# Performance work log

Measured on AMD Instinct MI355X. Metric: run time of the kernel, lower is better.

The kernel has to match this reference:

```python
import jax, jax.numpy as jnp
import numpy as np

GMIN, GMAX = 0.1, 1.0
DIMS = [3, 256, 256, 256, 1]

def setup_inputs() -> dict:
    key = jax.random.key(0)
    ks = jax.random.split(key, 12)
    inp = {"pos": jax.random.normal(ks[0], (1048576, 3), dtype=jnp.float32)}
    for i in range(4):
        fan_in = DIMS[i]
        bound = 1.0 / np.sqrt(fan_in)
        inp[f"W{i}"] = jax.random.uniform(ks[1 + 2 * i], (fan_in, DIMS[i + 1]), jnp.float32, -bound, bound)
        inp[f"b{i}"] = jax.random.uniform(ks[2 + 2 * i], (DIMS[i + 1],), jnp.float32, -bound, bound)
    for i in range(3):
        inp[f"sigma{i}"] = jax.random.uniform(ks[9 + i], (256,), jnp.float32, GMIN, GMAX)
    return inp

def _gauss(x, sigma):
    # Gaussian activation: exp(-x^2 / (2*sigma^2)), sigma learnable per-feature
    return jnp.exp(-jnp.square(x) / (2.0 * jnp.square(sigma)))

def _softplus8(x):
    # torch Softplus(beta=1, threshold=8): linear beyond threshold
    return jnp.where(x > 8.0, x, jnp.log1p(jnp.exp(jnp.minimum(x, 8.0))))

def reference(pos, W0, b0, W1, b1, W2, b2, W3, b3, sigma0, sigma1, sigma2):
    h = _gauss(pos @ W0 + b0, sigma0)      # [N,256]
    h = _gauss(h @ W1 + b1, sigma1)        # [N,256]
    h = _gauss(h @ W2 + b2, sigma2)        # [N,256]
    return _softplus8(h @ W3 + b3)         # [N,1]
```

## Files before the change

### kernel.cpp

```cpp
#include <hip/hip_runtime.h>
#include <hip/hip_bf16.h>

typedef __attribute__((ext_vector_type(8))) short short8;
typedef __attribute__((ext_vector_type(4))) float f32x4;
typedef __attribute__((ext_vector_type(2))) float f32x2;
typedef __attribute__((ext_vector_type(2))) unsigned int uint2v;

#define LOG2E 1.4426950408889634f
#define LN2   0.6931471805599453f

__device__ __forceinline__ unsigned short f2bf(float f) {
    union { float f; unsigned u; } v; v.f = f;
    unsigned u = v.u;
    u += 0x7fffu + ((u >> 16) & 1u);
    return (unsigned short)(u >> 16);
}
__device__ __forceinline__ float bf2f(unsigned short h) {
    union { unsigned u; float f; } v; v.u = ((unsigned)h) << 16;
    return v.f;
}
__device__ __forceinline__ unsigned pk_bf16(float a, float b) {
    __hip_bfloat162 t = __float22bfloat162_rn(float2{a, b});
    union { __hip_bfloat162 b; unsigned u; } v; v.b = t;
    return v.u;
}
__device__ __forceinline__ f32x2 pk_fma2(f32x2 a, f32x2 b, f32x2 c) {
    f32x2 d;
    asm("v_pk_fma_f32 %0, %1, %2, %3" : "=v"(d) : "v"(a), "v"(b), "v"(c));
    return d;
}

__global__ void pack_kernel(const float* __restrict__ W0, const float* __restrict__ W1,
                            const float* __restrict__ W2, const float* __restrict__ W3,
                            const float* __restrict__ s0, const float* __restrict__ s1,
                            const float* __restrict__ s2,
                            const float* __restrict__ b0, const float* __restrict__ b1,
                            const float* __restrict__ b2,
                            unsigned short* __restrict__ wp, float* __restrict__ negc) {
    int tid = blockIdx.x * 256 + threadIdx.x;
    if (tid < 8192) {
        int j = tid & 7, lane = (tid >> 3) & 63, ct = (tid >> 9) & 3, w = tid >> 11;
        int k = ((lane >> 4) * 8) + j;
        int n = w * 64 + 4 * (lane & 15) + ct;
        unsigned short v = 0;
        if (k < 9) {
            int d = k / 3, m = k - d * 3;
            float wv = W0[d * 256 + n];
            unsigned short wh = f2bf(wv);
            v = (m == 1) ? f2bf(wv - bf2f(wh)) : wh;
        }
        wp[tid] = v;
    } else if (tid < 139264) {
        int e = tid - 8192;
        const float* W = W1;
        if (e >= 65536) { W = W2; e -= 65536; }
        int j = e & 7, lane = (e >> 3) & 63, ct = (e >> 9) & 3, ks = (e >> 11) & 7, w = e >> 14;
        int k = ks * 32 + ((lane >> 4) * 8) + j;
        int n = w * 64 + 4 * (lane & 15) + ct;
        wp[tid] = f2bf(W[k * 256 + n]);
    } else if (tid < 143360) {
        int e = tid - 139264;
        int j = e & 7, lane = (e >> 3) & 63, ks = (e >> 9) & 1, w = e >> 10;
        int i16p = lane & 15, qp = lane >> 4;
        int k = w * 64 + ks * 32 + qp * 8 + j;
        float wv = W3[k];
        unsigned short wh = f2bf(wv);
        unsigned short v = 0;
        if (i16p == 0) v = wh;
        else if (i16p == 1) v = f2bf(wv - bf2f(wh));
        wp[139264 + e] = v;
    }
    if (tid < 768) {
        int l = tid >> 8, n = tid & 255;
        const float* s = (l == 0) ? s0 : (l == 1 ? s1 : s2);
        const float* b = (l == 0) ? b0 : (l == 1 ? b1 : b2);
        float sv = s[n], bv = b[n];
        float np = -LOG2E / (2.0f * sv * sv);
        negc[l * 768 + n]       = np;
        negc[l * 768 + 256 + n] = 2.0f * np * bv;
        negc[l * 768 + 512 + n] = np * bv * bv;
    }
}

constexpr int ROWS = 64;
constexpr int HSTR = 264;
constexpr int ASTR = 40;

template <int NKS, int SSTR>
__device__ __forceinline__ void layer(const unsigned short* __restrict__ src,
                                      const unsigned short* __restrict__ wpk,
                                      const float* __restrict__ ncp,
                                      unsigned short* __restrict__ hdst,
                                      int w, int i16, int q, bool presync) {
    f32x4 acc[4][4];
#pragma unroll
    for (int rg = 0; rg < 4; ++rg)
#pragma unroll
        for (int ct = 0; ct < 4; ++ct)
            acc[rg][ct] = f32x4{0.f, 0.f, 0.f, 0.f};

    const int lane = q * 16 + i16;
    const short8* wp8 = (const short8*)wpk + (w * NKS * 4) * 64 + lane;
    const unsigned short* abase = src + i16 * SSTR + q * 8;

    short8 wbufA[4], wbufB[4];
#pragma unroll
    for (int ct = 0; ct < 4; ++ct) wbufA[ct] = wp8[ct * 64];

#pragma unroll
    for (int ks = 0; ks < NKS; ++ks) {
        if (ks + 1 < NKS) {
#pragma unroll
            for (int ct = 0; ct < 4; ++ct) {
                short8 t = wp8[((ks + 1) * 4 + ct) * 64];
                if (ks & 1) wbufA[ct] = t; else wbufB[ct] = t;
            }
        }
        short8 a[4];
#pragma unroll
        for (int rg = 0; rg < 4; ++rg)
            a[rg] = *(const short8*)(abase + rg * 16 * SSTR + ks * 32);
#pragma unroll
        for (int ct = 0; ct < 4; ++ct) {
            short8 wf = (ks & 1) ? wbufB[ct] : wbufA[ct];
#pragma unroll
            for (int rg = 0; rg < 4; ++rg)
                acc[rg][ct] = __builtin_amdgcn_mfma_f32_16x16x32_bf16(a[rg], wf, acc[rg][ct], 0, 0, 0);
        }
    }

    const int ce = w * 64 + 4 * i16;
    const f32x4 np = *(const f32x4*)(ncp + ce);
    const f32x4 C1 = *(const f32x4*)(ncp + 256 + ce);
    const f32x4 C2 = *(const f32x4*)(ncp + 512 + ce);
    f32x2 npb[4], c1b[4], c2b[4];
#pragma unroll
    for (int ct = 0; ct < 4; ++ct) {
        npb[ct] = f32x2{np[ct], np[ct]};
        c1b[ct] = f32x2{C1[ct], C1[ct]};
        c2b[ct] = f32x2{C2[ct], C2[ct]};
    }
    uint2v av[4][4];
#pragma unroll
    for (int rg = 0; rg < 4; ++rg) {
        float gg[4][4];
#pragma unroll
        for (int ct = 0; ct < 4; ++ct) {
            f32x2 xlo = f32x2{acc[rg][ct][0], acc[rg][ct][1]};
            f32x2 xhi = f32x2{acc[rg][ct][2], acc[rg][ct][3]};
            f32x2 ulo = pk_fma2(npb[ct], xlo, c1b[ct]);
            f32x2 uhi = pk_fma2(npb[ct], xhi, c1b[ct]);
            f32x2 ylo = pk_fma2(ulo, xlo, c2b[ct]);
            f32x2 yhi = pk_fma2(uhi, xhi, c2b[ct]);
            gg[0][ct] = __builtin_amdgcn_exp2f(ylo[0]);
            gg[1][ct] = __builtin_amdgcn_exp2f(ylo[1]);
            gg[2][ct] = __builtin_amdgcn_exp2f(yhi[0]);
            gg[3][ct] = __builtin_amdgcn_exp2f(yhi[1]);
        }
#pragma unroll
        for (int rr = 0; rr < 4; ++rr) {
            uint2v v;
            v[0] = pk_bf16(gg[rr][0], gg[rr][1]);
            v[1] = pk_bf16(gg[rr][2], gg[rr][3]);
            av[rg][rr] = v;
        }
    }
    if (presync) __syncthreads();
#pragma unroll
    for (int rg = 0; rg < 4; ++rg) {
        int rbase = rg * 16 + q * 4;
#pragma unroll
        for (int rr = 0; rr < 4; ++rr)
            *(uint2v*)&hdst[(rbase + rr) * HSTR + ce] = av[rg][rr];
    }
    __syncthreads();
}

__global__ __launch_bounds__(256, 3) void mlp_kernel(
    const float* __restrict__ pos,
    const float* __restrict__ b3,
    const unsigned short* __restrict__ Wp,
    const float* __restrict__ negc,
    float* __restrict__ out)
{
    __shared__ unsigned short h[ROWS * HSTR];
    __shared__ unsigned short A0[ROWS * ASTR];

    const int tid  = threadIdx.x;
    const int lane = tid & 63;
    const int wave = tid >> 6;
    const int i16  = lane & 15, q = lane >> 4;
    const long row0 = (long)blockIdx.x * ROWS;

    if (tid < ROWS) {
        const float* pp = pos + (row0 + tid) * 3;
        float p0 = pp[0], p1 = pp[1], p2 = pp[2];
        short h0 = (short)f2bf(p0); short l0 = (short)f2bf(p0 - bf2f((unsigned short)h0));
        short h1 = (short)f2bf(p1); short l1 = (short)f2bf(p1 - bf2f((unsigned short)h1));
        short h2 = (short)f2bf(p2); short l2 = (short)f2bf(p2 - bf2f((unsigned short)h2));
        unsigned short* arow = A0 + tid * ASTR;
        *(short8*)(arow + 0)  = short8{h0, h0, l0, h1, h1, l1, h2, h2};
        *(short8*)(arow + 8)  = short8{l2, 0, 0, 0, 0, 0, 0, 0};
        *(short8*)(arow + 16) = short8{0, 0, 0, 0, 0, 0, 0, 0};
        *(short8*)(arow + 24) = short8{0, 0, 0, 0, 0, 0, 0, 0};
    }
    __syncthreads();

    layer<1, ASTR>(A0, Wp,         negc,        h, wave, i16, q, false);
    layer<8, HSTR>(h,  Wp + 8192,  negc + 768,  h, wave, i16, q, true);
    layer<8, HSTR>(h,  Wp + 73728, negc + 1536, h, wave, i16, q, true);

    {
        const short8* w3p = (const short8*)(Wp + 139264) + (wave * 2) * 64 + lane;
        const unsigned short* ab3 = h + i16 * HSTR + wave * 64 + q * 8;
        f32x4 acc3[4];
#pragma unroll
        for (int rg = 0; rg < 4; ++rg) acc3[rg] = f32x4{0.f, 0.f, 0.f, 0.f};
#pragma unroll
        for (int ks = 0; ks < 2; ++ks) {
            short8 wf = w3p[ks * 64];
#pragma unroll
            for (int rg = 0; rg < 4; ++rg) {
                short8 a = *(const short8*)(ab3 + rg * 16 * HSTR + ks * 32);
                acc3[rg] = __builtin_amdgcn_mfma_f32_16x16x32_bf16(a, wf, acc3[rg], 0, 0, 0);
            }
        }
        float* scr = (float*)A0;
        if (i16 < 2) {
#pragma unroll
            for (int rg = 0; rg < 4; ++rg)
                *(f32x4*)&scr[(wave * 2 + i16) * 64 + rg * 16 + q * 4] = acc3[rg];
        }
        __syncthreads();
        if (tid < 64) {
            float s = 0.f;
#pragma unroll
            for (int g = 0; g < 8; ++g) s += scr[g * 64 + tid];
            float x  = s + b3[0];
            float xm = fminf(x, 8.0f);
            float e  = __builtin_amdgcn_exp2f(xm * LOG2E);
            float sp = __builtin_amdgcn_logf(1.0f + e) * LN2;
            out[row0 + tid] = (x > 8.0f) ? x : sp;
        }
    }
}

extern "C" void kernel_launch(void* const* d_in, const int* in_sizes, int n_in,
                              void* d_out, int out_size, void* d_ws, size_t ws_size,
                              hipStream_t stream) {
    const float* pos = (const float*)d_in[0];
    const float* W0  = (const float*)d_in[1];
    const float* b0  = (const float*)d_in[2];
    const float* W1  = (const float*)d_in[3];
    const float* b1  = (const float*)d_in[4];
    const float* W2  = (const float*)d_in[5];
    const float* b2  = (const float*)d_in[6];
    const float* W3  = (const float*)d_in[7];
    const float* b3  = (const float*)d_in[8];
    const float* s0  = (const float*)d_in[9];
    const float* s1  = (const float*)d_in[10];
    const float* s2  = (const float*)d_in[11];

    unsigned short* wp = (unsigned short*)d_ws;
    float* negc = (float*)((char*)d_ws + 286720);

    pack_kernel<<<560, 256, 0, stream>>>(W0, W1, W2, W3, s0, s1, s2, b0, b1, b2, wp, negc);

    int nrows = in_sizes[0] / 3;
    int nblk  = nrows / ROWS;
    mlp_kernel<<<nblk, 256, 0, stream>>>(pos, b3, wp, negc,
                                         (float*)d_out);
}
```

Measured before the change: 400.3 us.

## Fold Gaussian sigma scale into weights, drop weight prefetch, raise occupancy

Precomputes sqrt(log2e/(2σ²)) and folds it into the packed bf16 weights and bias, so the epilogue becomes add, square, exp2 instead of two FMAs with three per-column constants. It also removes the explicit double-buffered weight register prefetch and raises launch bounds from 3 to 4 blocks per CU to cut register pressure and increase occupancy. Scaling weights before bf16 rounding changes the rounding error slightly, and losing the prefetch can expose global load latency inside the MFMA loop.

```diff
diff --git a/kernel.cpp b/kernel.cpp
--- a/kernel.cpp
+++ b/kernel.cpp
@@ -1,5 +1,6 @@
 #include <hip/hip_runtime.h>
 #include <hip/hip_bf16.h>
+#include <math.h>
 
 typedef __attribute__((ext_vector_type(8))) short short8;
 typedef __attribute__((ext_vector_type(4))) float f32x4;
@@ -24,9 +25,14 @@
     union { __hip_bfloat162 b; unsigned u; } v; v.b = t;
     return v.u;
 }
-__device__ __forceinline__ f32x2 pk_fma2(f32x2 a, f32x2 b, f32x2 c) {
+__device__ __forceinline__ f32x2 pk_add2(f32x2 a, f32x2 b) {
     f32x2 d;
-    asm("v_pk_fma_f32 %0, %1, %2, %3" : "=v"(d) : "v"(a), "v"(b), "v"(c));
+    asm("v_pk_add_f32 %0, %1, %2" : "=v"(d) : "v"(a), "v"(b));
+    return d;
+}
+__device__ __forceinline__ f32x2 pk_mul2(f32x2 a, f32x2 b) {
+    f32x2 d;
+    asm("v_pk_mul_f32 %0, %1, %2" : "=v"(d) : "v"(a), "v"(b));
     return d;
 }
 
@@ -45,7 +51,9 @@
         unsigned short v = 0;
         if (k < 9) {
             int d = k / 3, m = k - d * 3;
-            float wv = W0[d * 256 + n];
+            float sv = s0[n];
+            float sc = sqrtf(LOG2E / (2.0f * sv * sv));
+            float wv = W0[d * 256 + n] * sc;
             unsigned short wh = f2bf(wv);
             v = (m == 1) ? f2bf(wv - bf2f(wh)) : wh;
         }
@@ -53,11 +61,14 @@
     } else if (tid < 139264) {
         int e = tid - 8192;
         const float* W = W1;
-        if (e >= 65536) { W = W2; e -= 65536; }
+        const float* S = s1;
+        if (e >= 65536) { W = W2; S = s2; e -= 65536; }
         int j = e & 7, lane = (e >> 3) & 63, ct = (e >> 9) & 3, ks = (e >> 11) & 7, w = e >> 14;
         int k = ks * 32 + ((lane >> 4) * 8) + j;
         int n = w * 64 + 4 * (lane & 15) + ct;
-        wp[tid] = f2bf(W[k * 256 + n]);
+        float sv = S[n];
+        float sc = sqrtf(LOG2E / (2.0f * sv * sv));
+        wp[tid] = f2bf(W[k * 256 + n] * sc);
     } else if (tid < 143360) {
         int e = tid - 139264;
         int j = e & 7, lane = (e >> 3) & 63, ks = (e >> 9) & 1, w = e >> 10;
@@ -75,10 +86,8 @@
         const float* s = (l == 0) ? s0 : (l == 1 ? s1 : s2);
         const float* b = (l == 0) ? b0 : (l == 1 ? b1 : b2);
         float sv = s[n], bv = b[n];
-        float np = -LOG2E / (2.0f * sv * sv);
-        negc[l * 768 + n]       = np;
-        negc[l * 768 + 256 + n] = 2.0f * np * bv;
-        negc[l * 768 + 512 + n] = np * bv * bv;
+        float sc = sqrtf(LOG2E / (2.0f * sv * sv));
+        negc[l * 256 + n] = sc * bv;
     }
 }
 
@@ -103,26 +112,15 @@
     const short8* wp8 = (const short8*)wpk + (w * NKS * 4) * 64 + lane;
     const unsigned short* abase = src + i16 * SSTR + q * 8;
 
-    short8 wbufA[4], wbufB[4];
-#pragma unroll
-    for (int ct = 0; ct < 4; ++ct) wbufA[ct] = wp8[ct * 64];
-
 #pragma unroll
     for (int ks = 0; ks < NKS; ++ks) {
-        if (ks + 1 < NKS) {
-#pragma unroll
-            for (int ct = 0; ct < 4; ++ct) {
-                short8 t = wp8[((ks + 1) * 4 + ct) * 64];
-                if (ks & 1) wbufA[ct] = t; else wbufB[ct] = t;
-            }
-        }
         short8 a[4];
 #pragma unroll
         for (int rg = 0; rg < 4; ++rg)
             a[rg] = *(const short8*)(abase + rg * 16 * SSTR + ks * 32);
 #pragma unroll
         for (int ct = 0; ct < 4; ++ct) {
-            short8 wf = (ks & 1) ? wbufB[ct] : wbufA[ct];
+            short8 wf = wp8[(ks * 4 + ct) * 64];
 #pragma unroll
             for (int rg = 0; rg < 4; ++rg)
                 acc[rg][ct] = __builtin_amdgcn_mfma_f32_16x16x32_bf16(a[rg], wf, acc[rg][ct], 0, 0, 0);
@@ -130,16 +128,10 @@
     }
 
     const int ce = w * 64 + 4 * i16;
-    const f32x4 np = *(const f32x4*)(ncp + ce);
-    const f32x4 C1 = *(const f32x4*)(ncp + 256 + ce);
-    const f32x4 C2 = *(const f32x4*)(ncp + 512 + ce);
-    f32x2 npb[4], c1b[4], c2b[4];
-#pragma unroll
-    for (int ct = 0; ct < 4; ++ct) {
-        npb[ct] = f32x2{np[ct], np[ct]};
-        c1b[ct] = f32x2{C1[ct], C1[ct]};
-        c2b[ct] = f32x2{C2[ct], C2[ct]};
-    }
+    const f32x4 T = *(const f32x4*)(ncp + ce);
+    f32x2 tb[4];
+#pragma unroll
+    for (int ct = 0; ct < 4; ++ct) tb[ct] = f32x2{T[ct], T[ct]};
     uint2v av[4][4];
 #pragma unroll
     for (int rg = 0; rg < 4; ++rg) {
@@ -148,14 +140,14 @@
         for (int ct = 0; ct < 4; ++ct) {
             f32x2 xlo = f32x2{acc[rg][ct][0], acc[rg][ct][1]};
             f32x2 xhi = f32x2{acc[rg][ct][2], acc[rg][ct][3]};
-            f32x2 ulo = pk_fma2(npb[ct], xlo, c1b[ct]);
-            f32x2 uhi = pk_fma2(npb[ct], xhi, c1b[ct]);
-            f32x2 ylo = pk_fma2(ulo, xlo, c2b[ct]);
-            f32x2 yhi = pk_fma2(uhi, xhi, c2b[ct]);
-            gg[0][ct] = __builtin_amdgcn_exp2f(ylo[0]);
-            gg[1][ct] = __builtin_amdgcn_exp2f(ylo[1]);
-            gg[2][ct] = __builtin_amdgcn_exp2f(yhi[0]);
-            gg[3][ct] = __builtin_amdgcn_exp2f(yhi[1]);
+            f32x2 ylo = pk_add2(xlo, tb[ct]);
+            f32x2 yhi = pk_add2(xhi, tb[ct]);
+            f32x2 wlo = pk_mul2(ylo, ylo);
+            f32x2 whi = pk_mul2(yhi, yhi);
+            gg[0][ct] = __builtin_amdgcn_exp2f(-wlo[0]);
+            gg[1][ct] = __builtin_amdgcn_exp2f(-wlo[1]);
+            gg[2][ct] = __builtin_amdgcn_exp2f(-whi[0]);
+            gg[3][ct] = __builtin_amdgcn_exp2f(-whi[1]);
         }
 #pragma unroll
         for (int rr = 0; rr < 4; ++rr) {
@@ -176,7 +168,7 @@
     __syncthreads();
 }
 
-__global__ __launch_bounds__(256, 3) void mlp_kernel(
+__global__ __launch_bounds__(256, 4) void mlp_kernel(
     const float* __restrict__ pos,
     const float* __restrict__ b3,
     const unsigned short* __restrict__ Wp,
@@ -207,8 +199,8 @@
     __syncthreads();
 
     layer<1, ASTR>(A0, Wp,         negc,        h, wave, i16, q, false);
-    layer<8, HSTR>(h,  Wp + 8192,  negc + 768,  h, wave, i16, q, true);
-    layer<8, HSTR>(h,  Wp + 73728, negc + 1536, h, wave, i16, q, true);
+    layer<8, HSTR>(h,  Wp + 8192,  negc + 256,  h, wave, i16, q, true);
+    layer<8, HSTR>(h,  Wp + 73728, negc + 512,  h, wave, i16, q, true);
 
     {
         const short8* w3p = (const short8*)(Wp + 139264) + (wave * 2) * 64 + lane;
```

Measured after the change: 376.4 us. 6.0% less time.
